# Optimization experiments

Hardware: AMD Instinct MI355X
Metric: run time of the kernel (lower is better)

Reference implementation:

```python
import jax, jax.numpy as jnp
import numpy as np

# Static module config (from Encoder's CropConv layers)
B, CIN, COUT, H, W = 32, 256, 256, 64, 64
K, STRIDE, PAD, DIL = 3, 2, 1, 1
OVERLAP, CENTER = 0, 4


def _build_crop_mask(in_h, out_h, out_w, center_size, overlap):
    """Faithful replica of CropConv's python-loop mask construction,
    including python-slice clamping to L = out_h*out_w."""
    L = out_h * out_w
    crop_start = (in_h - in_h // center_size) // 2 - overlap
    start_idx = in_h * crop_start + crop_start
    crop_size = in_h // center_size + overlap * 2
    not_cropped = crop_start * 2

    def seg_len(a, b):
        # length of python slice [a:b] on an array of length L
        return max(0, min(b, L) - min(a, L))

    segs = []
    for i in range(crop_size):
        if i == 0:
            segs.append(np.ones(seg_len(0, start_idx), bool))
        if i == crop_size - 1:
            segs.append(np.zeros(seg_len(start_idx, start_idx + crop_size), bool))
            segs.append(np.ones(seg_len(start_idx + crop_size, in_h * in_h), bool))
            break
        segs.append(np.zeros(seg_len(start_idx, start_idx + crop_size), bool))
        segs.append(np.ones(seg_len(start_idx + crop_size, start_idx + not_cropped), bool))
        start_idx += in_h
    mask = np.concatenate(segs)
    assert mask.shape[0] == L, (mask.shape[0], L)
    return mask.reshape(out_h, out_w)


def setup_inputs() -> dict:
    key = jax.random.key(0)
    kx, kw = jax.random.split(key)
    x = jax.random.normal(kx, (B, CIN, H, W), dtype=jnp.float32)
    # kaiming_normal(mode='fan_out', nonlinearity='relu'): std = sqrt(2 / (COUT*K*K))
    std = np.sqrt(2.0 / (COUT * K * K)).astype(np.float32)
    weight = jax.random.normal(kw, (COUT, CIN, K, K), dtype=jnp.float32) * std
    return {"x": x, "weight": weight}


def reference(x, weight):
    out_h = (H - K + 2 * PAD) // STRIDE + 1
    out_w = (W - K + 2 * PAD) // STRIDE + 1
    # unfold + matmul == standard convolution; use the efficient fused form
    out = jax.lax.conv_general_dilated(
        x, weight,
        window_strides=(STRIDE, STRIDE),
        padding=[(PAD, PAD), (PAD, PAD)],
        rhs_dilation=(DIL, DIL),
        dimension_numbers=("NCHW", "OIHW", "NCHW"))  # [B, COUT, out_h, out_w]
    mask = jnp.asarray(_build_crop_mask(H, out_h, out_w, CENTER, OVERLAP))
    return jnp.where(mask[None, None, :, :], out, jnp.float32(0.0))
```

## Files before the change

kernel.cpp:

```cpp
#include <hip/hip_runtime.h>


#define B_   32
#define CIN  256
#define COUT 256
#define H_   64
#define W_   64
#define OH   32
#define OW   32

typedef _Float16 f16;
typedef _Float16 half8 __attribute__((ext_vector_type(8)));
typedef float    floatx16 __attribute__((ext_vector_type(16)));

__global__ __launch_bounds__(256) void repack_w_kernel(const float* __restrict__ w,
                                                       f16* __restrict__ rp) {
  int o = blockIdx.x * 256 + threadIdx.x;
  int ci_l = o & 15;
  int tt = o >> 4;
  int co_l = tt & 127; tt >>= 7;
  int khw = tt % 9;    tt /= 9;
  int cc   = tt & 15;  tt >>= 4;
  int co_t = tt;
  int co = co_t * 128 + co_l;
  int ci = cc * 16 + ci_l;
  rp[o] = (f16)w[(co * CIN + ci) * 9 + khw];
}

#define XSP   (9 * 33 * 16)
#define XSP1  (XSP + 8)
#define XSBUF (XSP1 + XSP)

__global__ __launch_bounds__(256, 2) void conv_mfma_kernel(
    const float* __restrict__ x, const f16* __restrict__ rp,
    float* __restrict__ out) {
  __shared__ f16 ws[9 * 128 * 16];
  __shared__ f16 xs[2 * XSBUF];

  const int t    = threadIdx.x;
  const int lane = t & 63;
  const int wave = t >> 6;
  const int wm   = wave >> 1;
  const int wn   = wave & 1;

  const int blk  = blockIdx.x;
  const int b    = blk >> 4;
  const int rem  = blk & 15;
  const int co_t = rem >> 3;
  const int oh0  = (rem & 7) << 2;
  const int ih0  = 2 * oh0 - 1;

  const float* xb  = x + (size_t)b * CIN * H_ * W_;
  const f16*   rpb = rp + (size_t)co_t * (16 * 9 * 128 * 16);

  const int iw    = t & 63;
  const int rr    = t >> 6;
  const int k0    = (lane >> 5) * 8;
  const int ml    = lane & 31;
  const int p_st  = iw & 1;
  const int idx_st = (iw + p_st) >> 1;

  floatx16 acc[2][2];
#pragma unroll
  for (int mi = 0; mi < 2; ++mi)
#pragma unroll
    for (int nj = 0; nj < 2; ++nj)
#pragma unroll
      for (int i = 0; i < 16; ++i) acc[mi][nj][i] = 0.f;

  float xv[3][2][8];
  half8 wv[9];

  auto load_x = [&](int cc) {
#pragma unroll
    for (int it = 0; it < 3; ++it) {
      const int r = rr + it * 4;
      if (r < 9) {
        const int ih = ih0 + r;
        if (ih >= 0) {
          const float* xp = xb + (size_t)cc * 16 * (H_ * W_) + (size_t)ih * W_ + iw;
#pragma unroll
          for (int g = 0; g < 2; ++g)
#pragma unroll
            for (int c = 0; c < 8; ++c)
              xv[it][g][c] = xp[(size_t)(g * 8 + c) * (H_ * W_)];
        } else {
#pragma unroll
          for (int g = 0; g < 2; ++g)
#pragma unroll
            for (int c = 0; c < 8; ++c) xv[it][g][c] = 0.f;
        }
      }
    }
  };

  auto load_w = [&](int cc) {
    const half8* src = (const half8*)(rpb + cc * (9 * 128 * 16));
#pragma unroll
    for (int i = 0; i < 9; ++i) wv[i] = src[t + i * 256];
  };

  auto write_x = [&](int nxt) {
    f16* xd = &xs[nxt * XSBUF + (p_st ? XSP1 : 0)];
#pragma unroll
    for (int it = 0; it < 3; ++it) {
      const int r = rr + it * 4;
      if (r < 9) {
#pragma unroll
        for (int g = 0; g < 2; ++g) {
          half8 v;
#pragma unroll
          for (int c = 0; c < 8; ++c) v[c] = (f16)xv[it][g][c];
          *(half8*)&xd[(r * 33 + idx_st) * 16 + g * 8] = v;
        }
      }
    }
  };

  auto write_w = [&]() {
    half8* dst = (half8*)ws;
#pragma unroll
    for (int i = 0; i < 9; ++i) dst[t + i * 256] = wv[i];
  };

  auto compute = [&](int cur) {
    const f16* xc = &xs[cur * XSBUF];
    __builtin_amdgcn_s_setprio(1);
#pragma unroll
    for (int kh = 0; kh < 3; ++kh) {
#pragma unroll
      for (int kw = 0; kw < 3; ++kw) {
        const int khw = kh * 3 + kw;
        half8 a0 = *(const half8*)&ws[(khw * 128 + wm * 64 + ml) * 16 + k0];
        half8 a1 = *(const half8*)&ws[(khw * 128 + wm * 64 + 32 + ml) * 16 + k0];
        const int pp  = (kw & 1) ^ 1;
        const int idx = ml + (kw >> 1);
        const f16* xpl = xc + (pp ? XSP1 : 0);
#pragma unroll
        for (int nj = 0; nj < 2; ++nj) {
          const int r = 2 * (wn * 2 + nj) + kh;
          half8 bf = *(const half8*)&xpl[(r * 33 + idx) * 16 + k0];
          acc[0][nj] = __builtin_amdgcn_mfma_f32_32x32x16_f16(a0, bf, acc[0][nj], 0, 0, 0);
          acc[1][nj] = __builtin_amdgcn_mfma_f32_32x32x16_f16(a1, bf, acc[1][nj], 0, 0, 0);
        }
      }
    }
    __builtin_amdgcn_s_setprio(0);
  };

  if (t < 144) {
    const int r = t >> 4, ci = t & 15;
    xs[0 * XSBUF + XSP1 + (r * 33) * 16 + ci] = (f16)0.f;
    xs[1 * XSBUF + XSP1 + (r * 33) * 16 + ci] = (f16)0.f;
  }

  load_x(0);
  load_w(0);
  write_x(0);
  write_w();
  __syncthreads();

  int cur = 0;
#pragma unroll 1
  for (int cc = 0; cc < 15; ++cc) {
    load_x(cc + 1);
    load_w(cc + 1);
    __builtin_amdgcn_sched_barrier(0);
    compute(cur);
    write_x(cur ^ 1);
    __syncthreads();
    write_w();
    __syncthreads();
    cur ^= 1;
  }
  compute(cur);

  const int col = ml;
  const int rowbase = (lane >> 5) * 4;
  float* ob = out + ((size_t)b * COUT + co_t * 128 + wm * 64) * (OH * OW);
#pragma unroll
  for (int mi = 0; mi < 2; ++mi) {
#pragma unroll
    for (int nj = 0; nj < 2; ++nj) {
      const int oh = oh0 + wn * 2 + nj;
#pragma unroll
      for (int r = 0; r < 16; ++r) {
        const int row = mi * 32 + (r & 3) + 8 * (r >> 2) + rowbase;
        ob[(size_t)row * (OH * OW) + oh * OW + col] = acc[mi][nj][r];
      }
    }
  }
}

extern "C" void kernel_launch(void* const* d_in, const int* in_sizes, int n_in,
                              void* d_out, int out_size, void* d_ws, size_t ws_size,
                              hipStream_t stream) {
  const float* x = (const float*)d_in[0];
  const float* w = (const float*)d_in[1];
  float* out = (float*)d_out;
  f16* rp = (f16*)d_ws;

  repack_w_kernel<<<2304, 256, 0, stream>>>(w, rp);
  conv_mfma_kernel<<<512, 256, 0, stream>>>(x, rp, out);
}
```

Baseline: 221.7 us.

## Deepen prefetch pipeline with dual x register sets and XOR-swizzled LDS

Prefetches input two channel-chunks ahead using two register buffers, unrolls the main loop by two so the LDS buffers are fixed pointers, and replaces __syncthreads with a custom barrier that waits only on LDS counters so global loads stay in flight across barriers. LDS writes and reads for both weights and activations use an XOR swizzle on the 8-half group to cut bank conflicts. The aim is to hide global memory latency behind the MFMA work. In exchange it needs more VGPRs for the extra prefetch buffer, which may reduce occupancy under launch_bounds(256,2).

```diff
diff --git a/kernel.cpp b/kernel.cpp
--- a/kernel.cpp
+++ b/kernel.cpp
@@ -27,15 +27,18 @@
   rp[o] = (f16)w[(co * CIN + ci) * 9 + khw];
 }
 
-#define XSP   (9 * 33 * 16)
-#define XSP1  (XSP + 8)
-#define XSBUF (XSP1 + XSP)
+static __device__ __forceinline__ void wg_barrier() {
+  __builtin_amdgcn_sched_barrier(0);
+  asm volatile("s_waitcnt lgkmcnt(0)" ::: "memory");
+  __builtin_amdgcn_s_barrier();
+  __builtin_amdgcn_sched_barrier(0);
+}
 
 __global__ __launch_bounds__(256, 2) void conv_mfma_kernel(
     const float* __restrict__ x, const f16* __restrict__ rp,
     float* __restrict__ out) {
-  __shared__ f16 ws[9 * 128 * 16];
-  __shared__ f16 xs[2 * XSBUF];
+  __shared__ __align__(16) f16 ws[18432];
+  __shared__ __align__(16) f16 xs[19040];
 
   const int t    = threadIdx.x;
   const int lane = t & 63;
@@ -53,12 +56,16 @@
   const float* xb  = x + (size_t)b * CIN * H_ * W_;
   const f16*   rpb = rp + (size_t)co_t * (16 * 9 * 128 * 16);
 
-  const int iw    = t & 63;
-  const int rr    = t >> 6;
-  const int k0    = (lane >> 5) * 8;
-  const int ml    = lane & 31;
-  const int p_st  = iw & 1;
+  const int iw  = t & 63;
+  const int rru = __builtin_amdgcn_readfirstlane(t >> 6);
+  const int k0  = (lane >> 5) * 8;
+  const int ml  = lane & 31;
+  const int p_st   = iw & 1;
   const int idx_st = (iw + p_st) >> 1;
+  const int gx     = (idx_st >> 3) & 1;
+
+  f16* const xs0 = xs;
+  f16* const xs1 = xs + 9520;
 
   floatx16 acc[2][2];
 #pragma unroll
@@ -68,22 +75,23 @@
 #pragma unroll
       for (int i = 0; i < 16; ++i) acc[mi][nj][i] = 0.f;
 
-  float xv[3][2][8];
+  float xva[3][2][8], xvb[3][2][8];
   half8 wv[9];
 
-  auto load_x = [&](int cc) {
+  auto load_x = [&](float (&xv)[3][2][8], int cc) {
+    const float* bcc = xb + (size_t)cc * 16 * 4096;
 #pragma unroll
     for (int it = 0; it < 3; ++it) {
-      const int r = rr + it * 4;
+      const int r = rru + it * 4;
       if (r < 9) {
         const int ih = ih0 + r;
         if (ih >= 0) {
-          const float* xp = xb + (size_t)cc * 16 * (H_ * W_) + (size_t)ih * W_ + iw;
+          const float* p0 = bcc + (size_t)ih * 64 + iw;
 #pragma unroll
           for (int g = 0; g < 2; ++g)
 #pragma unroll
             for (int c = 0; c < 8; ++c)
-              xv[it][g][c] = xp[(size_t)(g * 8 + c) * (H_ * W_)];
+              xv[it][g][c] = p0[(size_t)(g * 8 + c) * 4096];
         } else {
 #pragma unroll
           for (int g = 0; g < 2; ++g)
@@ -95,51 +103,53 @@
   };
 
   auto load_w = [&](int cc) {
-    const half8* src = (const half8*)(rpb + cc * (9 * 128 * 16));
+    const half8* src = (const half8*)(rpb + (size_t)cc * 18432);
 #pragma unroll
     for (int i = 0; i < 9; ++i) wv[i] = src[t + i * 256];
   };
 
-  auto write_x = [&](int nxt) {
-    f16* xd = &xs[nxt * XSBUF + (p_st ? XSP1 : 0)];
+  auto write_x = [&](float (&xv)[3][2][8], f16* xoth) {
+    f16* d = xoth + p_st * 4760 + idx_st * 16;
 #pragma unroll
     for (int it = 0; it < 3; ++it) {
-      const int r = rr + it * 4;
+      const int r = rru + it * 4;
       if (r < 9) {
 #pragma unroll
         for (int g = 0; g < 2; ++g) {
           half8 v;
 #pragma unroll
           for (int c = 0; c < 8; ++c) v[c] = (f16)xv[it][g][c];
-          *(half8*)&xd[(r * 33 + idx_st) * 16 + g * 8] = v;
+          *(half8*)&d[r * 528 + (g ^ gx) * 8] = v;
         }
       }
     }
   };
 
+  const int colw = (t >> 1) & 127;
+  f16* const wdst = ws + colw * 16 + (((t & 1) * 8) ^ (colw & 8));
   auto write_w = [&]() {
-    half8* dst = (half8*)ws;
-#pragma unroll
-    for (int i = 0; i < 9; ++i) dst[t + i * 256] = wv[i];
-  };
-
-  auto compute = [&](int cur) {
-    const f16* xc = &xs[cur * XSBUF];
+#pragma unroll
+    for (int i = 0; i < 9; ++i) *(half8*)&wdst[i * 2048] = wv[i];
+  };
+
+  const f16* const Aw = ws + wm * 1024 + ml * 16 + (k0 ^ (ml & 8));
+
+  auto compute = [&](const f16* xcur) {
+    const f16* Be  = xcur + wn * 2112 + ml * 16 + (k0 ^ (ml & 8));
+    const f16* Bo1 = Be + 4760;
+    const f16* Bo2 = xcur + 4760 + wn * 2112 + (ml + 1) * 16 + (k0 ^ ((ml + 1) & 8));
     __builtin_amdgcn_s_setprio(1);
 #pragma unroll
     for (int kh = 0; kh < 3; ++kh) {
 #pragma unroll
       for (int kw = 0; kw < 3; ++kw) {
         const int khw = kh * 3 + kw;
-        half8 a0 = *(const half8*)&ws[(khw * 128 + wm * 64 + ml) * 16 + k0];
-        half8 a1 = *(const half8*)&ws[(khw * 128 + wm * 64 + 32 + ml) * 16 + k0];
-        const int pp  = (kw & 1) ^ 1;
-        const int idx = ml + (kw >> 1);
-        const f16* xpl = xc + (pp ? XSP1 : 0);
+        half8 a0 = *(const half8*)&Aw[khw * 2048];
+        half8 a1 = *(const half8*)&Aw[khw * 2048 + 512];
+        const f16* Bp = (kw == 0) ? Bo1 : (kw == 1) ? Be : Bo2;
 #pragma unroll
         for (int nj = 0; nj < 2; ++nj) {
-          const int r = 2 * (wn * 2 + nj) + kh;
-          half8 bf = *(const half8*)&xpl[(r * 33 + idx) * 16 + k0];
+          half8 bf = *(const half8*)&Bp[nj * 1056 + kh * 528];
           acc[0][nj] = __builtin_amdgcn_mfma_f32_32x32x16_f16(a0, bf, acc[0][nj], 0, 0, 0);
           acc[1][nj] = __builtin_amdgcn_mfma_f32_32x32x16_f16(a1, bf, acc[1][nj], 0, 0, 0);
         }
@@ -150,30 +160,36 @@
 
   if (t < 144) {
     const int r = t >> 4, ci = t & 15;
-    xs[0 * XSBUF + XSP1 + (r * 33) * 16 + ci] = (f16)0.f;
-    xs[1 * XSBUF + XSP1 + (r * 33) * 16 + ci] = (f16)0.f;
+    xs0[4760 + r * 528 + ci] = (f16)0.f;
+    xs1[4760 + r * 528 + ci] = (f16)0.f;
   }
 
-  load_x(0);
-  load_w(0);
-  write_x(0);
+  load_x(xva, 0); load_w(0);
+  write_x(xva, xs0);
   write_w();
+  load_x(xva, 1);
+  load_x(xvb, 2);
+  load_w(1);
   __syncthreads();
 
-  int cur = 0;
 #pragma unroll 1
-  for (int cc = 0; cc < 15; ++cc) {
-    load_x(cc + 1);
-    load_w(cc + 1);
-    __builtin_amdgcn_sched_barrier(0);
-    compute(cur);
-    write_x(cur ^ 1);
-    __syncthreads();
+  for (int cc = 0; cc < 16; cc += 2) {
+    compute(xs0);
+    write_x(xva, xs1);
+    if (cc + 3 < 16) load_x(xva, cc + 3);
+    wg_barrier();
     write_w();
-    __syncthreads();
-    cur ^= 1;
+    if (cc + 2 < 16) load_w(cc + 2);
+    wg_barrier();
+
+    compute(xs1);
+    if (cc + 2 < 16) write_x(xvb, xs0);
+    if (cc + 4 < 16) load_x(xvb, cc + 4);
+    wg_barrier();
+    if (cc + 2 < 16) write_w();
+    if (cc + 3 < 16) load_w(cc + 3);
+    wg_barrier();
   }
-  compute(cur);
 
   const int col = ml;
   const int rowbase = (lane >> 5) * 4;
```

New measurement: 225.1 us. No clear change (+1.6%).
